# Kernel optimization log

Hardware: AMD Instinct MI355X
Metric: run time of the kernel (lower is better)

Reference implementation:

```python
import jax, jax.numpy as jnp
import numpy as np

B, T, EMB, H, LAT = 8192, 30, 128, 256, 256
DT = 0.03


def _lin(k, din, dout):
    k1, k2 = jax.random.split(k)
    s = 1.0 / np.sqrt(din)
    W = jax.random.uniform(k1, (din, dout), minval=-s, maxval=s, dtype=jnp.float32)
    b = jax.random.uniform(k2, (dout,), minval=-s, maxval=s, dtype=jnp.float32)
    return W, b


def setup_inputs():
    key = jax.random.key(0)
    ks = list(jax.random.split(key, 32))
    inp = {}
    inp['expert_traj'] = jax.random.normal(ks[0], (B, T, 4), dtype=jnp.float32)
    inp['init_state'] = jax.random.normal(ks[1], (B, 4), dtype=jnp.float32)
    inp['eps'] = jax.random.normal(ks[2], (B, LAT), dtype=jnp.float32)
    # encoder params
    inp['enc_emb_W'], inp['enc_emb_b'] = _lin(ks[3], 4, EMB)
    inp['enc_Wih'], inp['enc_bih'] = _lin(ks[4], EMB, 4 * H)
    inp['enc_Whh'], inp['enc_bhh'] = _lin(ks[5], H, 4 * H)
    # mu / log_var MLPs: 4 layers, all HxH since latent==h
    muW, mub, lvW, lvb = [], [], [], []
    for i in range(4):
        W, b = _lin(ks[6 + i], H, H); muW.append(W); mub.append(b)
        W, b = _lin(ks[10 + i], H, H); lvW.append(W); lvb.append(b)
    inp['mu_W'] = jnp.stack(muW); inp['mu_b'] = jnp.stack(mub)
    inp['lv_W'] = jnp.stack(lvW); inp['lv_b'] = jnp.stack(lvb)
    # decoder params
    inp['dec_emb_W'], inp['dec_emb_b'] = _lin(ks[14], 4, EMB)
    inp['dec_init_W'], inp['dec_init_b'] = _lin(ks[15], LAT, H)
    inp['dec_Wih'], inp['dec_bih'] = _lin(ks[16], EMB, 4 * H)
    inp['dec_Whh'], inp['dec_bhh'] = _lin(ks[17], H, 4 * H)
    inp['ctrl_W'], inp['ctrl_b'] = _lin(ks[18], H, 2)
    return inp


def _lstm_cell(x, h, c, Wih, Whh, bih, bhh):
    g = x @ Wih + bih + h @ Whh + bhh            # [B, 4H]
    i, f, gg, o = jnp.split(g, 4, axis=-1)       # torch gate order i,f,g,o
    i = jax.nn.sigmoid(i); f = jax.nn.sigmoid(f)
    gg = jnp.tanh(gg); o = jax.nn.sigmoid(o)
    c = f * c + i * gg
    return o * jnp.tanh(c), c


def reference(expert_traj, init_state, eps,
              enc_emb_W, enc_emb_b, enc_Wih, enc_bih, enc_Whh, enc_bhh,
              mu_W, mu_b, lv_W, lv_b,
              dec_emb_W, dec_emb_b, dec_init_W, dec_init_b,
              dec_Wih, dec_bih, dec_Whh, dec_bhh, ctrl_W, ctrl_b):
    # ---- encoder: relative positions ----
    rel_xy = jnp.concatenate([expert_traj[:, :1, :2],
                              expert_traj[:, 1:, :2] - expert_traj[:, :-1, :2]], axis=1)
    rel = jnp.concatenate([rel_xy, expert_traj[:, :, 2:]], axis=2)  # [B,T,4]
    emb = rel @ enc_emb_W + enc_emb_b                               # [B,T,EMB]
    xs = jnp.swapaxes(emb, 0, 1)                                    # [T,B,EMB]

    def enc_step(carry, x):
        h, c = carry
        h, c = _lstm_cell(x, h, c, enc_Wih, enc_Whh, enc_bih, enc_bhh)
        return (h, c), None
    h0 = jnp.zeros((expert_traj.shape[0], H), dtype=expert_traj.dtype)
    (h_enc, _), _ = jax.lax.scan(enc_step, (h0, h0), xs)

    mu, lv = h_enc, h_enc
    for i in range(4):
        mu = jax.nn.leaky_relu(mu @ mu_W[i] + mu_b[i])
        lv = jax.nn.leaky_relu(lv @ lv_W[i] + lv_b[i])

    # ---- reparameterize + tanh ----
    z = jnp.tanh(eps * jnp.exp(0.5 * lv) + mu)                      # [B,LAT]

    # ---- decoder ----
    hd = z @ dec_init_W + dec_init_b                                # [B,H]

    def dec_step(carry, _):
        h, c, s = carry
        x = s @ dec_emb_W + dec_emb_b
        h, c = _lstm_cell(x, h, c, dec_Wih, dec_Whh, dec_bih, dec_bhh)
        ctrl = h @ ctrl_W + ctrl_b                                  # [B,2]
        pedal = ctrl[:, 0]
        steer = jnp.clip(ctrl[:, 1], -0.5, 0.5)
        x_t, y_t, psi, v = s[:, 0], s[:, 1], s[:, 2], s[:, 3]
        v1 = jnp.clip(v + pedal * DT, 0.0, 10.0)
        psi_dot = jnp.clip(v * jnp.tan(steer) / 2.5, -3.14 / 2, 3.14 / 2)
        s_new = jnp.stack([x_t + v1 * jnp.cos(psi) * DT,
                           y_t + v1 * jnp.sin(psi) * DT,
                           psi + psi_dot * DT,
                           v1], axis=1)
        return (h, c, s_new), s_new

    _, traj = jax.lax.scan(dec_step, (hd, hd, init_state), None, length=T)
    recons = jnp.swapaxes(traj, 0, 1)                               # [B,T,4]
    return recons, expert_traj, mu, lv
```

## Files before the change

kernel.cpp:

```cpp
#include <hip/hip_runtime.h>
#include <math.h>

#define B_ 8192
#define T_ 30
#define H_ 256
#define NG_ 1024
#define DT_ 0.03f
#define RB 32
#define NBLK (B_ / RB)

typedef __attribute__((ext_vector_type(8))) short short8;
typedef __attribute__((ext_vector_type(4))) float f32x4;
typedef __attribute__((ext_vector_type(4))) int i32x4;

__device__ inline float bf2f(unsigned short u) {
    unsigned int x = ((unsigned int)u) << 16;
    return __builtin_bit_cast(float, x);
}
__device__ inline unsigned short f2bf(float f) {
    unsigned int x = __builtin_bit_cast(unsigned int, f);
    return (unsigned short)((x + 0x7FFF + ((x >> 16) & 1)) >> 16);
}
__device__ inline float fast_tanh(float x) {
    float e = __expf(2.f * x);
    return 1.f - 2.f / (e + 1.f);
}
__device__ inline float fast_sigmoid(float x) {
    return 1.f / (1.f + __expf(-x));
}
__device__ inline void gl16(const signed char* g, signed char* l) {
    __builtin_amdgcn_global_load_lds((const __attribute__((address_space(1))) void*)g,
                                     (__attribute__((address_space(3))) void*)l, 16, 0, 0);
}

__global__ void fold_perm_kernel(const float* __restrict__ W1, const float* __restrict__ b1,
                                 const float* __restrict__ W2,
                                 const float* __restrict__ bih, const float* __restrict__ bhh,
                                 float* __restrict__ WxP, float* __restrict__ bfP) {
    __shared__ float sP[4][64];
    const int t63 = threadIdx.x & 63;
    const int kc = threadIdx.x >> 6;
    int o = blockIdx.x * 64 + t63;
    int r = o >> 10;
    int np = o & 1023;
    int bN = np >> 6, g = (np >> 4) & 3, j = np & 15;
    int co = g * 256 + bN * 16 + j;
    const float* w1row = (r < 4) ? (W1 + r * 128) : b1;
    float acc = 0.f;
    #pragma unroll 8
    for (int k = kc * 32; k < kc * 32 + 32; ++k)
        acc = fmaf(w1row[k], W2[k * NG_ + co], acc);
    sP[kc][t63] = acc;
    __syncthreads();
    if (kc == 0) {
        acc = sP[0][t63] + sP[1][t63] + sP[2][t63] + sP[3][t63];
        if (r < 4) WxP[r * NG_ + np] = acc;
        else       bfP[np] = acc + bih[co] + bhh[co];
    }
}

__global__ void prep_pack_i8_kernel(const float* __restrict__ W, signed char* __restrict__ Wpk) {
    int id = blockIdx.x * blockDim.x + threadIdx.x;
    int np = id >> 8, k = id & 255;
    int bN = np >> 6, gg = (np >> 4) & 3, j = np & 15;
    int co = gg * 256 + bN * 16 + j;
    int colgrp = np >> 4, fr = np & 15;
    int k0 = k >> 5, kg = (k >> 3) & 3, e = k & 7;
    float q = rintf(W[(size_t)k * NG_ + co] * 2032.f);
    q = fminf(fmaxf(q, -127.f), 127.f);
    Wpk[colgrp * 4096 + k0 * 512 + kg * 128 + fr * 8 + e] = (signed char)q;
}

__global__ void prep_wt_all_kernel(const float* __restrict__ muW, const float* __restrict__ lvW,
                                   const float* __restrict__ diW, unsigned short* __restrict__ WT9) {
    int m = blockIdx.y;
    const float* src = (m < 4) ? muW + (size_t)m * 65536
                     : (m < 8) ? lvW + (size_t)(m - 4) * 65536
                               : diW;
    int id = blockIdx.x * 256 + threadIdx.x;
    int n = id >> 8, k = id & 255;
    WT9[(size_t)m * 65536 + id] = f2bf(src[k * H_ + n]);
}

__global__ void rel_kernel(const float* __restrict__ traj, float* __restrict__ rel,
                           float4* __restrict__ expert) {
    int id = blockIdx.x * blockDim.x + threadIdx.x;
    if (id >= B_ * T_) return;
    int t = id % T_;
    const float* p = traj + (size_t)id * 4;
    float x = p[0], y = p[1];
    if (t > 0) { x -= p[-4]; y -= p[-3]; }
    float* o = rel + (size_t)id * 4;
    o[0] = x; o[1] = y; o[2] = p[2]; o[3] = p[3];
    expert[id] = ((const float4*)traj)[id];
}

#define SMEM15 150528

template <int DEC>
__global__ __launch_bounds__(512, 2) void lstm_persist15_kernel(
    const float* __restrict__ rel,
    const signed char* __restrict__ Wpk,
    const float* __restrict__ WxP,
    const float* __restrict__ bfP,
    const float* __restrict__ cInit,
    const unsigned short* __restrict__ hInit,
    const float* __restrict__ initS,
    const float* __restrict__ Wc,
    const float* __restrict__ bc,
    unsigned short* __restrict__ hOut,
    float* __restrict__ recons)
{
    extern __shared__ char smem[];
    signed char* bufs = (signed char*)smem;
    signed char* hL   = (signed char*)(smem + 131072);
    float* sLp  = (float*)(smem + 147968);
    float* redL = (float*)(smem + 148480);

    const int tid = threadIdx.x;
    const int lane = tid & 63;
    const int fr = lane & 15;
    const int kg = lane >> 4;
    const int w = tid >> 6;
    const int rh = w >> 2;
    const int cq = w & 3;
    const int rowBase = blockIdx.x * RB;

    float wxR[4][4][4], bfR[4][4], wcR[4][2];
    float cReg[16];
    #pragma unroll
    for (int c = 0; c < 4; ++c) {
        const int np0 = c * 256 + cq * 64 + fr;
        const int u = (c * 4 + cq) * 16 + fr;
        #pragma unroll
        for (int g = 0; g < 4; ++g) bfR[c][g] = bfP[np0 + g * 16];
        #pragma unroll
        for (int k = 0; k < 4; ++k)
            #pragma unroll
            for (int g = 0; g < 4; ++g)
                wxR[c][k][g] = WxP[k * 1024 + np0 + g * 16];
        if (DEC) { wcR[c][0] = Wc[u * 2]; wcR[c][1] = Wc[u * 2 + 1]; }
        else     { wcR[c][0] = 0.f; wcR[c][1] = 0.f; }
        #pragma unroll
        for (int rr = 0; rr < 4; ++rr) {
            if (DEC) cReg[c * 4 + rr] =
                cInit[(size_t)(rowBase + rh * 16 + kg * 4 + rr) * 256 + u];
            else cReg[c * 4 + rr] = 0.f;
        }
    }

    {
        int row = tid >> 4, sb = tid & 15;
        signed char* dst = hL + row * 264 + sb * 16;
        if (DEC) {
            const unsigned short* src = hInit + (size_t)(rowBase + row) * 256 + sb * 16;
            #pragma unroll
            for (int i = 0; i < 16; ++i) {
                float h = bf2f(src[i]);
                h = fminf(fmaxf(h, -4.f), 4.f);
                dst[i] = (signed char)(int)rintf(h * 31.75f);
            }
        } else {
            *(long*)(dst) = 0L;
            *(long*)(dst + 8) = 0L;
        }
    }
    if (DEC) {
        if (tid < RB) *(float4*)(sLp + tid * 4) = *(const float4*)(initS + (size_t)(rowBase + tid) * 4);
    }
    float bc0 = 0.f, bc1 = 0.f;
    if (DEC && tid < RB) { bc0 = bc[0]; bc1 = bc[1]; }

    #define STAGE(ck, bp)                                                          \
        {                                                                          \
            const signed char* gsrc = Wpk + (ck) * 65536 + w * 8192 + lane * 16;   \
            signed char* ldst = bufs + (bp) * 65536 + w * 8192 + lane * 16;        \
            _Pragma("unroll")                                                      \
            for (int q_ = 0; q_ < 8; ++q_) gl16(gsrc + q_ * 1024, ldst + q_ * 1024); \
        }

    STAGE(0, 0);
    STAGE(1, 1);
    __syncthreads();

    for (int t = 0; t < T_; ++t) {
        signed char* rbuf = hL + (t & 1) * 8448;
        signed char* wbuf = hL + ((t + 1) & 1) * 8448;
        const float dqA = (DEC && t == 0) ? (4.f / 258064.f) : (1.f / 258064.f);

        long afr[8];
        float4 xv[4];
        float p0[4], p1[4];
        if (DEC) {
            #pragma unroll
            for (int i = 0; i < 4; ++i) { p0[i] = 0.f; p1[i] = 0.f; }
        }

        #pragma unroll
        for (int c = 0; c < 4; ++c) {
            signed char* bufc = bufs + (c & 1) * 65536;
            if (t == T_ - 1 && c == 3) asm volatile("s_waitcnt vmcnt(0)" ::: "memory");
            else                       asm volatile("s_waitcnt vmcnt(8)" ::: "memory");
            asm volatile("s_waitcnt lgkmcnt(0)" ::: "memory");
            __builtin_amdgcn_s_barrier();
            __builtin_amdgcn_sched_barrier(0);

            if (c == 0) {
                #pragma unroll
                for (int k0 = 0; k0 < 8; ++k0)
                    afr[k0] = *(const long*)(rbuf + (rh * 16 + fr) * 264 + (k0 * 4 + kg) * 8);
                #pragma unroll
                for (int rr = 0; rr < 4; ++rr) {
                    int row = rh * 16 + kg * 4 + rr;
                    if (DEC) xv[rr] = *(const float4*)(sLp + row * 4);
                    else     xv[rr] = *(const float4*)(rel + ((size_t)(rowBase + row) * T_ + t) * 4);
                }
            }

            i32x4 acc[4] = {};
            __builtin_amdgcn_s_setprio(1);
            #pragma unroll
            for (int k0 = 0; k0 < 8; ++k0) {
                long b0 = *(const long*)(bufc + (cq * 4 + 0) * 4096 + k0 * 512 + lane * 8);
                long b1 = *(const long*)(bufc + (cq * 4 + 1) * 4096 + k0 * 512 + lane * 8);
                long b2 = *(const long*)(bufc + (cq * 4 + 2) * 4096 + k0 * 512 + lane * 8);
                long b3 = *(const long*)(bufc + (cq * 4 + 3) * 4096 + k0 * 512 + lane * 8);
                acc[0] = __builtin_amdgcn_mfma_i32_16x16x32_i8(afr[k0], b0, acc[0], 0, 0, 0);
                acc[1] = __builtin_amdgcn_mfma_i32_16x16x32_i8(afr[k0], b1, acc[1], 0, 0, 0);
                acc[2] = __builtin_amdgcn_mfma_i32_16x16x32_i8(afr[k0], b2, acc[2], 0, 0, 0);
                acc[3] = __builtin_amdgcn_mfma_i32_16x16x32_i8(afr[k0], b3, acc[3], 0, 0, 0);
            }
            __builtin_amdgcn_s_setprio(0);
            asm volatile("s_waitcnt lgkmcnt(0)" ::: "memory");
            __builtin_amdgcn_sched_barrier(0);
            __builtin_amdgcn_s_barrier();
            if (!(t == T_ - 1 && c >= 2)) STAGE((c + 2) & 3, (c & 1));

            const int u = (c * 4 + cq) * 16 + fr;
            #pragma unroll
            for (int rr = 0; rr < 4; ++rr) {
                int row = rh * 16 + kg * 4 + rr;
                float xk[4] = {xv[rr].x, xv[rr].y, xv[rr].z, xv[rr].w};
                float g0 = fmaf((float)acc[0][rr], dqA, bfR[c][0]);
                float g1 = fmaf((float)acc[1][rr], dqA, bfR[c][1]);
                float g2 = fmaf((float)acc[2][rr], dqA, bfR[c][2]);
                float g3 = fmaf((float)acc[3][rr], dqA, bfR[c][3]);
                #pragma unroll
                for (int k = 0; k < 4; ++k) {
                    g0 = fmaf(xk[k], wxR[c][k][0], g0);
                    g1 = fmaf(xk[k], wxR[c][k][1], g1);
                    g2 = fmaf(xk[k], wxR[c][k][2], g2);
                    g3 = fmaf(xk[k], wxR[c][k][3], g3);
                }
                float iv = fast_sigmoid(g0);
                float fv = fast_sigmoid(g1);
                float gv = fast_tanh(g2);
                float ov = fast_sigmoid(g3);
                float cn = fv * cReg[c * 4 + rr] + iv * gv;
                cReg[c * 4 + rr] = cn;
                float hval = ov * fast_tanh(cn);
                if (DEC) {
                    p0[rr] = fmaf(hval, wcR[c][0], p0[rr]);
                    p1[rr] = fmaf(hval, wcR[c][1], p1[rr]);
                }
                wbuf[row * 264 + u] = (signed char)(int)rintf(hval * 127.f);
            }
        }

        if (DEC) {
            #pragma unroll
            for (int msk = 1; msk < 16; msk <<= 1)
                #pragma unroll
                for (int i = 0; i < 4; ++i) {
                    p0[i] += __shfl_xor(p0[i], msk);
                    p1[i] += __shfl_xor(p1[i], msk);
                }
            if (fr == 0) {
                #pragma unroll
                for (int rr = 0; rr < 4; ++rr) {
                    int row = rh * 16 + kg * 4 + rr;
                    redL[(row * 4 + cq) * 2 + 0] = p0[rr];
                    redL[(row * 4 + cq) * 2 + 1] = p1[rr];
                }
            }
            asm volatile("s_waitcnt lgkmcnt(0)" ::: "memory");
            __builtin_amdgcn_s_barrier();
            if (tid < RB) {
                float q0 = 0.f, q1 = 0.f;
                #pragma unroll
                for (int p = 0; p < 4; ++p) {
                    q0 += redL[(tid * 4 + p) * 2 + 0];
                    q1 += redL[(tid * 4 + p) * 2 + 1];
                }
                float pedal = q0 + bc0;
                float steer = fminf(fmaxf(q1 + bc1, -0.5f), 0.5f);
                float4 sv = *(float4*)(sLp + tid * 4);
                float v = sv.w;
                float v1 = fminf(fmaxf(v + pedal * DT_, 0.f), 10.f);
                float pd = fminf(fmaxf(v * tanf(steer) * (1.f / 2.5f), -1.57f), 1.57f);
                float4 ns;
                ns.x = sv.x + v1 * cosf(sv.z) * DT_;
                ns.y = sv.y + v1 * sinf(sv.z) * DT_;
                ns.z = sv.z + pd * DT_;
                ns.w = v1;
                *(float4*)(sLp + tid * 4) = ns;
                *(float4*)(recons + ((size_t)(rowBase + tid) * T_ + t) * 4) = ns;
            }
        }
    }

    if (!DEC) {
        asm volatile("s_waitcnt lgkmcnt(0)" ::: "memory");
        __builtin_amdgcn_s_barrier();
        int row = tid >> 4, sb = tid & 15;
        const signed char* src = hL + (T_ & 1) * 8448 + row * 264 + sb * 16;
        unsigned short hv[16];
        #pragma unroll
        for (int i = 0; i < 16; ++i)
            hv[i] = f2bf((float)src[i] * (1.f / 127.f));
        unsigned short* dst = hOut + (size_t)(rowBase + row) * 256 + sb * 16;
        *(short8*)(dst) = *(short8*)(hv);
        *(short8*)(dst + 8) = *(short8*)(hv + 8);
    }
    #undef STAGE
}

__global__ __launch_bounds__(256) void mlp_gemm_kernel(
    const unsigned short* __restrict__ Ain, size_t aZStride,
    const unsigned short* __restrict__ WTb, size_t wZStride,
    const float* __restrict__ b0, const float* __restrict__ b1,
    float* __restrict__ outF, size_t ofZStride,
    unsigned short* __restrict__ outB, size_t obZStride,
    int act)
{
    const int z = blockIdx.z;
    const unsigned short* A  = Ain + (size_t)z * aZStride;
    const unsigned short* WT = WTb + (size_t)z * wZStride;
    const float* bias = z ? b1 : b0;

    __shared__ __align__(16) short sA[64 * 256];
    __shared__ __align__(16) short sBm[64 * 256];
    const int tid = threadIdx.x;
    const int lane = tid & 63;
    const int wr = (tid >> 7) & 1;
    const int wc = (tid >> 6) & 1;
    const int rowBase = blockIdx.x * 64;
    const int nBase = blockIdx.y * 64;

    {
        const unsigned short* gA = A + (size_t)rowBase * 256;
        const unsigned short* gB = WT + (size_t)nBase * 256;
        #pragma unroll
        for (int i = 0; i < 8; ++i) {
            int ch = tid + i * 256;
            int row = ch >> 5, slot = ch & 31;
            float4 va = *(const float4*)(gA + row * 256 + slot * 8);
            float4 vb = *(const float4*)(gB + row * 256 + slot * 8);
            int sl = slot ^ (row & 7);
            *(float4*)(sA + row * 256 + sl * 8) = va;
            *(float4*)(sBm + row * 256 + sl * 8) = vb;
        }
    }
    __syncthreads();

    const int fr = lane & 15;
    const int kg = lane >> 4;
    f32x4 acc[2][2] = {};
    #pragma unroll
    for (int k0 = 0; k0 < 8; ++k0) {
        int kch = k0 * 4 + kg;
        short8 a[2], b[2];
        #pragma unroll
        for (int m = 0; m < 2; ++m) {
            int r = wr * 32 + m * 16 + fr;
            a[m] = *(const short8*)(sA + r * 256 + (kch ^ (r & 7)) * 8);
        }
        #pragma unroll
        for (int n = 0; n < 2; ++n) {
            int r = wc * 32 + n * 16 + fr;
            b[n] = *(const short8*)(sBm + r * 256 + (kch ^ (r & 7)) * 8);
        }
        #pragma unroll
        for (int m = 0; m < 2; ++m)
            #pragma unroll
            for (int n = 0; n < 2; ++n)
                acc[m][n] = __builtin_amdgcn_mfma_f32_16x16x32_bf16(a[m], b[n], acc[m][n], 0, 0, 0);
    }

    #pragma unroll
    for (int m = 0; m < 2; ++m) {
        #pragma unroll
        for (int n = 0; n < 2; ++n) {
            int col = nBase + wc * 32 + n * 16 + fr;
            float bv = bias[col];
            #pragma unroll
            for (int r = 0; r < 4; ++r) {
                int row = rowBase + wr * 32 + m * 16 + kg * 4 + r;
                float v = acc[m][n][r] + bv;
                if (act) v = v > 0.f ? v : 0.01f * v;
                if (outF) outF[(size_t)z * ofZStride + (size_t)row * H_ + col] = v;
                if (outB) outB[(size_t)z * obZStride + (size_t)row * H_ + col] = f2bf(v);
            }
        }
    }
}

__global__ void z_kernel(const float* __restrict__ eps, const float* __restrict__ mu,
                         const float* __restrict__ lv, unsigned short* __restrict__ z) {
    int id = blockIdx.x * blockDim.x + threadIdx.x;
    z[id] = f2bf(tanhf(eps[id] * expf(0.5f * lv[id]) + mu[id]));
}

extern "C" void kernel_launch(void* const* d_in, const int* in_sizes, int n_in,
                              void* d_out, int out_size, void* d_ws, size_t ws_size,
                              hipStream_t stream) {
    (void)in_sizes; (void)n_in; (void)out_size; (void)ws_size;
    const float* traj       = (const float*)d_in[0];
    const float* init_s     = (const float*)d_in[1];
    const float* eps        = (const float*)d_in[2];
    const float* enc_emb_W  = (const float*)d_in[3];
    const float* enc_emb_b  = (const float*)d_in[4];
    const float* enc_Wih    = (const float*)d_in[5];
    const float* enc_bih    = (const float*)d_in[6];
    const float* enc_Whh    = (const float*)d_in[7];
    const float* enc_bhh    = (const float*)d_in[8];
    const float* mu_W       = (const float*)d_in[9];
    const float* mu_b       = (const float*)d_in[10];
    const float* lv_W       = (const float*)d_in[11];
    const float* lv_b       = (const float*)d_in[12];
    const float* dec_emb_W  = (const float*)d_in[13];
    const float* dec_emb_b  = (const float*)d_in[14];
    const float* dec_init_W = (const float*)d_in[15];
    const float* dec_init_b = (const float*)d_in[16];
    const float* dec_Wih    = (const float*)d_in[17];
    const float* dec_bih    = (const float*)d_in[18];
    const float* dec_Whh    = (const float*)d_in[19];
    const float* dec_bhh    = (const float*)d_in[20];
    const float* ctrl_W     = (const float*)d_in[21];
    const float* ctrl_b     = (const float*)d_in[22];

    float* out = (float*)d_out;
    float* recons = out;
    float* expert = out + (size_t)B_ * T_ * 4;
    float* mu_out = expert + (size_t)B_ * T_ * 4;
    float* lv_out = mu_out + (size_t)B_ * H_;

    float* ws = (float*)d_ws;
    size_t o = 0;
    float* rel = ws + o;  o += (size_t)B_ * T_ * 4;
    signed char* WpkE = (signed char*)(ws + o); o += NG_ * H_ / 4;
    signed char* WpkD = (signed char*)(ws + o); o += NG_ * H_ / 4;
    unsigned short* WT9  = (unsigned short*)(ws + o); o += 9 * H_ * H_ / 2;
    float* WxPE = ws + o; o += 4 * NG_;
    float* WxPD = ws + o; o += 4 * NG_;
    float* bfPE = ws + o; o += NG_;
    float* bfPD = ws + o; o += NG_;
    unsigned short* hEnc = (unsigned short*)(ws + o); o += (size_t)B_ * H_ / 2;
    unsigned short* tbA  = (unsigned short*)(ws + o); o += (size_t)B_ * H_;
    unsigned short* tbB  = (unsigned short*)(ws + o); o += (size_t)B_ * H_;
    float* cInit = ws + o; o += (size_t)B_ * H_;
    unsigned short* hInit = (unsigned short*)(ws + o); o += (size_t)B_ * H_ / 2;

    hipFuncSetAttribute((const void*)lstm_persist15_kernel<0>,
                        hipFuncAttributeMaxDynamicSharedMemorySize, SMEM15);
    hipFuncSetAttribute((const void*)lstm_persist15_kernel<1>,
                        hipFuncAttributeMaxDynamicSharedMemorySize, SMEM15);

    fold_perm_kernel<<<80, 256, 0, stream>>>(enc_emb_W, enc_emb_b, enc_Wih, enc_bih, enc_bhh, WxPE, bfPE);
    fold_perm_kernel<<<80, 256, 0, stream>>>(dec_emb_W, dec_emb_b, dec_Wih, dec_bih, dec_bhh, WxPD, bfPD);
    prep_pack_i8_kernel<<<1024, 256, 0, stream>>>(enc_Whh, WpkE);
    prep_pack_i8_kernel<<<1024, 256, 0, stream>>>(dec_Whh, WpkD);
    prep_wt_all_kernel<<<dim3(256, 9), 256, 0, stream>>>(mu_W, lv_W, dec_init_W, WT9);
    rel_kernel<<<(B_ * T_ + 255) / 256, 256, 0, stream>>>(traj, rel, (float4*)expert);

    lstm_persist15_kernel<0><<<NBLK, 512, SMEM15, stream>>>(
        rel, WpkE, WxPE, bfPE, nullptr, nullptr, nullptr, nullptr, nullptr, hEnc, nullptr);

    dim3 gridM2(B_ / 64, H_ / 64, 2);
    size_t BH = (size_t)B_ * H_;
    mlp_gemm_kernel<<<gridM2, 256, 0, stream>>>(hEnc, 0, WT9 + 0 * 65536, (size_t)4 * 65536,
                                                mu_b + 0,   lv_b + 0,   nullptr, 0, tbA, BH, 1);
    mlp_gemm_kernel<<<gridM2, 256, 0, stream>>>(tbA, BH, WT9 + 1 * 65536, (size_t)4 * 65536,
                                                mu_b + 256, lv_b + 256, nullptr, 0, tbB, BH, 1);
    mlp_gemm_kernel<<<gridM2, 256, 0, stream>>>(tbB, BH, WT9 + 2 * 65536, (size_t)4 * 65536,
                                                mu_b + 512, lv_b + 512, nullptr, 0, tbA, BH, 1);
    mlp_gemm_kernel<<<gridM2, 256, 0, stream>>>(tbA, BH, WT9 + 3 * 65536, (size_t)4 * 65536,
                                                mu_b + 768, lv_b + 768, mu_out, BH, nullptr, 0, 1);

    z_kernel<<<B_ * H_ / 256, 256, 0, stream>>>(eps, mu_out, lv_out, tbB);
    dim3 gridM1(B_ / 64, H_ / 64, 1);
    mlp_gemm_kernel<<<gridM1, 256, 0, stream>>>(tbB, 0, WT9 + 8 * 65536, 0,
                                                dec_init_b, dec_init_b, cInit, 0, hInit, 0, 0);

    lstm_persist15_kernel<1><<<NBLK, 512, SMEM15, stream>>>(
        nullptr, WpkD, WxPD, bfPD, cInit, hInit, init_s, ctrl_W, ctrl_b, nullptr, recons);
}
```

Baseline: 768.2 us.

## Halve LSTM rows per block and single-buffer weight chunks for two blocks per CU

Each persistent LSTM block now handles 16 batch rows with 4 waves instead of 32 rows with 8 waves. The weight chunk staging drops from double to single buffering, and the hidden-state LDS buffer from ping-pong to a single buffer. LDS per block falls from about 150KB to about 70KB, so two blocks can share a CU and hide each other's stalls. The cost is a full vmcnt(0) wait before every chunk, since loads no longer overlap with MFMA inside a block. Each block also streams the whole recurrent weight matrix for half as many rows, which doubles total weight traffic.

```diff
diff --git a/kernel.cpp b/kernel.cpp
--- a/kernel.cpp
+++ b/kernel.cpp
@@ -6,7 +6,7 @@
 #define H_ 256
 #define NG_ 1024
 #define DT_ 0.03f
-#define RB 32
+#define RB 16
 #define NBLK (B_ / RB)
 
 typedef __attribute__((ext_vector_type(8))) short short8;
@@ -95,10 +95,10 @@
     expert[id] = ((const float4*)traj)[id];
 }
 
-#define SMEM15 150528
+#define SMEM16 70528
 
 template <int DEC>
-__global__ __launch_bounds__(512, 2) void lstm_persist15_kernel(
+__global__ __launch_bounds__(256, 2) void lstm_persist16_kernel(
     const float* __restrict__ rel,
     const signed char* __restrict__ Wpk,
     const float* __restrict__ WxP,
@@ -112,18 +112,16 @@
     float* __restrict__ recons)
 {
     extern __shared__ char smem[];
-    signed char* bufs = (signed char*)smem;
-    signed char* hL   = (signed char*)(smem + 131072);
-    float* sLp  = (float*)(smem + 147968);
-    float* redL = (float*)(smem + 148480);
+    signed char* buf = (signed char*)smem;
+    signed char* hL  = (signed char*)(smem + 65536);
+    float* sLp  = (float*)(smem + 69760);
+    float* redL = (float*)(smem + 70016);
 
     const int tid = threadIdx.x;
     const int lane = tid & 63;
     const int fr = lane & 15;
     const int kg = lane >> 4;
-    const int w = tid >> 6;
-    const int rh = w >> 2;
-    const int cq = w & 3;
+    const int cq = tid >> 6;
     const int rowBase = blockIdx.x * RB;
 
     float wxR[4][4][4], bfR[4][4], wcR[4][2];
@@ -144,7 +142,7 @@
         #pragma unroll
         for (int rr = 0; rr < 4; ++rr) {
             if (DEC) cReg[c * 4 + rr] =
-                cInit[(size_t)(rowBase + rh * 16 + kg * 4 + rr) * 256 + u];
+                cInit[(size_t)(rowBase + kg * 4 + rr) * 256 + u];
             else cReg[c * 4 + rr] = 0.f;
         }
     }
@@ -171,21 +169,18 @@
     float bc0 = 0.f, bc1 = 0.f;
     if (DEC && tid < RB) { bc0 = bc[0]; bc1 = bc[1]; }
 
-    #define STAGE(ck, bp)                                                          \
-        {                                                                          \
-            const signed char* gsrc = Wpk + (ck) * 65536 + w * 8192 + lane * 16;   \
-            signed char* ldst = bufs + (bp) * 65536 + w * 8192 + lane * 16;        \
-            _Pragma("unroll")                                                      \
-            for (int q_ = 0; q_ < 8; ++q_) gl16(gsrc + q_ * 1024, ldst + q_ * 1024); \
-        }
-
-    STAGE(0, 0);
-    STAGE(1, 1);
+    #define STAGE(ck)                                                               \
+        {                                                                           \
+            const signed char* gsrc = Wpk + (ck) * 65536 + cq * 16384 + lane * 16;  \
+            signed char* ldst = buf + cq * 16384 + lane * 16;                       \
+            _Pragma("unroll")                                                       \
+            for (int q_ = 0; q_ < 16; ++q_) gl16(gsrc + q_ * 1024, ldst + q_ * 1024); \
+        }
+
+    STAGE(0);
     __syncthreads();
 
     for (int t = 0; t < T_; ++t) {
-        signed char* rbuf = hL + (t & 1) * 8448;
-        signed char* wbuf = hL + ((t + 1) & 1) * 8448;
         const float dqA = (DEC && t == 0) ? (4.f / 258064.f) : (1.f / 258064.f);
 
         long afr[8];
@@ -198,9 +193,7 @@
 
         #pragma unroll
         for (int c = 0; c < 4; ++c) {
-            signed char* bufc = bufs + (c & 1) * 65536;
-            if (t == T_ - 1 && c == 3) asm volatile("s_waitcnt vmcnt(0)" ::: "memory");
-            else                       asm volatile("s_waitcnt vmcnt(8)" ::: "memory");
+            asm volatile("s_waitcnt vmcnt(0)" ::: "memory");
             asm volatile("s_waitcnt lgkmcnt(0)" ::: "memory");
             __builtin_amdgcn_s_barrier();
             __builtin_amdgcn_sched_barrier(0);
@@ -208,10 +201,10 @@
             if (c == 0) {
                 #pragma unroll
                 for (int k0 = 0; k0 < 8; ++k0)
-                    afr[k0] = *(const long*)(rbuf + (rh * 16 + fr) * 264 + (k0 * 4 + kg) * 8);
+                    afr[k0] = *(const long*)(hL + fr * 264 + (k0 * 4 + kg) * 8);
                 #pragma unroll
                 for (int rr = 0; rr < 4; ++rr) {
-                    int row = rh * 16 + kg * 4 + rr;
+                    int row = kg * 4 + rr;
                     if (DEC) xv[rr] = *(const float4*)(sLp + row * 4);
                     else     xv[rr] = *(const float4*)(rel + ((size_t)(rowBase + row) * T_ + t) * 4);
                 }
@@ -221,10 +214,10 @@
             __builtin_amdgcn_s_setprio(1);
             #pragma unroll
             for (int k0 = 0; k0 < 8; ++k0) {
-                long b0 = *(const long*)(bufc + (cq * 4 + 0) * 4096 + k0 * 512 + lane * 8);
-                long b1 = *(const long*)(bufc + (cq * 4 + 1) * 4096 + k0 * 512 + lane * 8);
-                long b2 = *(const long*)(bufc + (cq * 4 + 2) * 4096 + k0 * 512 + lane * 8);
-                long b3 = *(const long*)(bufc + (cq * 4 + 3) * 4096 + k0 * 512 + lane * 8);
+                long b0 = *(const long*)(buf + (cq * 4 + 0) * 4096 + k0 * 512 + lane * 8);
+                long b1 = *(const long*)(buf + (cq * 4 + 1) * 4096 + k0 * 512 + lane * 8);
+                long b2 = *(const long*)(buf + (cq * 4 + 2) * 4096 + k0 * 512 + lane * 8);
+                long b3 = *(const long*)(buf + (cq * 4 + 3) * 4096 + k0 * 512 + lane * 8);
                 acc[0] = __builtin_amdgcn_mfma_i32_16x16x32_i8(afr[k0], b0, acc[0], 0, 0, 0);
                 acc[1] = __builtin_amdgcn_mfma_i32_16x16x32_i8(afr[k0], b1, acc[1], 0, 0, 0);
                 acc[2] = __builtin_amdgcn_mfma_i32_16x16x32_i8(afr[k0], b2, acc[2], 0, 0, 0);
@@ -234,12 +227,12 @@
             asm volatile("s_waitcnt lgkmcnt(0)" ::: "memory");
             __builtin_amdgcn_sched_barrier(0);
             __builtin_amdgcn_s_barrier();
-            if (!(t == T_ - 1 && c >= 2)) STAGE((c + 2) & 3, (c & 1));
+            if (!(t == T_ - 1 && c == 3)) STAGE((c + 1) & 3);
 
             const int u = (c * 4 + cq) * 16 + fr;
             #pragma unroll
             for (int rr = 0; rr < 4; ++rr) {
-                int row = rh * 16 + kg * 4 + rr;
+                int row = kg * 4 + rr;
                 float xk[4] = {xv[rr].x, xv[rr].y, xv[rr].z, xv[rr].w};
                 float g0 = fmaf((float)acc[0][rr], dqA, bfR[c][0]);
                 float g1 = fmaf((float)acc[1][rr], dqA, bfR[c][1]);
@@ -263,7 +256,7 @@
                     p0[rr] = fmaf(hval, wcR[c][0], p0[rr]);
                     p1[rr] = fmaf(hval, wcR[c][1], p1[rr]);
                 }
-                wbuf[row * 264 + u] = (signed char)(int)rintf(hval * 127.f);
+                hL[row * 264 + u] = (signed char)(int)rintf(hval * 127.f);
             }
         }
 
@@ -278,7 +271,7 @@
             if (fr == 0) {
                 #pragma unroll
                 for (int rr = 0; rr < 4; ++rr) {
-                    int row = rh * 16 + kg * 4 + rr;
+                    int row = kg * 4 + rr;
                     redL[(row * 4 + cq) * 2 + 0] = p0[rr];
                     redL[(row * 4 + cq) * 2 + 1] = p1[rr];
                 }
@@ -313,7 +306,7 @@
         asm volatile("s_waitcnt lgkmcnt(0)" ::: "memory");
         __builtin_amdgcn_s_barrier();
         int row = tid >> 4, sb = tid & 15;
-        const signed char* src = hL + (T_ & 1) * 8448 + row * 264 + sb * 16;
+        const signed char* src = hL + row * 264 + sb * 16;
         unsigned short hv[16];
         #pragma unroll
         for (int i = 0; i < 16; ++i)
@@ -461,10 +454,10 @@
     float* cInit = ws + o; o += (size_t)B_ * H_;
     unsigned short* hInit = (unsigned short*)(ws + o); o += (size_t)B_ * H_ / 2;
 
-    hipFuncSetAttribute((const void*)lstm_persist15_kernel<0>,
-                        hipFuncAttributeMaxDynamicSharedMemorySize, SMEM15);
-    hipFuncSetAttribute((const void*)lstm_persist15_kernel<1>,
-                        hipFuncAttributeMaxDynamicSharedMemorySize, SMEM15);
+    hipFuncSetAttribute((const void*)lstm_persist16_kernel<0>,
+                        hipFuncAttributeMaxDynamicSharedMemorySize, SMEM16);
+    hipFuncSetAttribute((const void*)lstm_persist16_kernel<1>,
+                        hipFuncAttributeMaxDynamicSharedMemorySize, SMEM16);
 
     fold_perm_kernel<<<80, 256, 0, stream>>>(enc_emb_W, enc_emb_b, enc_Wih, enc_bih, enc_bhh, WxPE, bfPE);
     fold_perm_kernel<<<80, 256, 0, stream>>>(dec_emb_W, dec_emb_b, dec_Wih, dec_bih, dec_bhh, WxPD, bfPD);
@@ -473,7 +466,7 @@
     prep_wt_all_kernel<<<dim3(256, 9), 256, 0, stream>>>(mu_W, lv_W, dec_init_W, WT9);
     rel_kernel<<<(B_ * T_ + 255) / 256, 256, 0, stream>>>(traj, rel, (float4*)expert);
 
-    lstm_persist15_kernel<0><<<NBLK, 512, SMEM15, stream>>>(
+    lstm_persist16_kernel<0><<<NBLK, 256, SMEM16, stream>>>(
         rel, WpkE, WxPE, bfPE, nullptr, nullptr, nullptr, nullptr, nullptr, hEnc, nullptr);
 
     dim3 gridM2(B_ / 64, H_ / 64, 2);
@@ -492,6 +485,6 @@
     mlp_gemm_kernel<<<gridM1, 256, 0, stream>>>(tbB, 0, WT9 + 8 * 65536, 0,
                                                 dec_init_b, dec_init_b, cInit, 0, hInit, 0, 0);
 
-    lstm_persist15_kernel<1><<<NBLK, 512, SMEM15, stream>>>(
+    lstm_persist16_kernel<1><<<NBLK, 256, SMEM16, stream>>>(
         nullptr, WpkD, WxPD, bfPD, cInit, hInit, init_s, ctrl_W, ctrl_b, nullptr, recons);
 }
```

Result: slower. 1.135 ms (+47.7%).
